# Performance work log

Hardware: AMD Instinct MI355X
Metric: run time of the kernel (lower is better)

The kernel has to match this reference:

```python
import jax, jax.numpy as jnp
import numpy as np

S, G, NMUL, LENF = 730, 4000, 2, 15
NEARZERO = 1e-5

# param bounds (change_param_range: lb + raw*(ub-lb)), raw in [0,1]
HBV_LB = np.array([1., 50., .05, .01, .001, .2, 0., 0., -2.5, .5, 0., 0.], np.float32)
HBV_UB = np.array([6., 1000., .9, .5, .2, 1., 10., 100., 2.5, 10., .1, .2], np.float32)
EXP_LB = np.array([0., 100., 10., 0., 0., -3.], np.float32)
EXP_UB = np.array([.1, 1500., 50., 5., 3., 0.], np.float32)


def _descale(raw, lb, ub):
    # raw: [G, n_par, NMUL]
    return lb[None, :, None] + raw * (ub - lb)[None, :, None]


def _hbv(P, T, PET, ph):
    # ph: [G,12,NMUL]; order: beta fc k0 k1 k2 lp perc uzl tt cfmax cfr cwh
    beta, fc, k0, k1, k2, lp, perc, uzl, tt, cfmax, cfr, cwh = [ph[:, i, :] for i in range(12)]

    def step(carry, inp):
        sp, mw, sm, suz, slz = carry
        p, t, pet = inp
        rain = jnp.where(t >= tt, p, 0.)
        sp = sp + jnp.where(t < tt, p, 0.)
        melt = jnp.minimum(jnp.maximum(cfmax * (t - tt), 0.), sp)
        mw = mw + melt; sp = sp - melt
        refr = jnp.minimum(jnp.maximum(cfr * cfmax * (tt - t), 0.), mw)
        sp = sp + refr; mw = mw - refr
        tosoil = jnp.maximum(mw - cwh * sp, 0.)
        mw = mw - tosoil
        sw = jnp.clip((sm / fc) ** beta, 0., 1.)
        rech = (rain + tosoil) * sw
        sm = sm + rain + tosoil - rech
        excess = jnp.maximum(sm - fc, 0.); sm = sm - excess
        et = jnp.minimum(pet * jnp.clip(sm / (lp * fc), 0., 1.), sm)
        sm = jnp.maximum(sm - et, NEARZERO)
        suz = suz + rech + excess
        pa = jnp.minimum(perc, suz); suz = suz - pa
        q0 = k0 * jnp.maximum(suz - uzl, 0.); suz = suz - q0
        q1 = k1 * suz; suz = suz - q1
        slz = slz + pa
        q2 = k2 * slz; slz = slz - q2
        return (sp, mw, sm, suz, slz), q0 + q1 + q2

    z = jnp.full_like(fc, NEARZERO)
    init = (z, z, 0.5 * fc, z, z)
    _, q = jax.lax.scan(step, init, (P, T, PET))
    return q  # [S,G,NMUL]


def _exphydro(P, T, PET, pe):
    # pe: [G,6,NMUL]; order: f smax qmax df tmax tmin
    f, smax, qmax, df, tmax, tmin = [pe[:, i, :] for i in range(6)]

    def step(carry, inp):
        s0, s1 = carry
        p, t, pet = inp
        ps = jnp.where(t <= tmin, p, 0.)
        pr = p - ps
        melt = jnp.where(t > tmax, jnp.minimum(s0, df * (t - tmax)), 0.)
        s0 = s0 + ps - melt
        s1 = s1 + pr + melt
        qspill = jnp.maximum(s1 - smax, 0.); s1 = s1 - qspill
        et = jnp.minimum(pet * jnp.clip(s1 / smax, 0., 1.), s1); s1 = s1 - et
        qb = jnp.minimum(qmax * jnp.exp(-f * jnp.maximum(smax - s1, 0.)), s1)
        s1 = s1 - qb
        return (s0, s1), qspill + qb

    z = jnp.full_like(smax, NEARZERO)
    init = (z, 0.5 * smax)
    _, q = jax.lax.scan(step, init, (P, T, PET))
    return q  # [S,G,NMUL]


def _uh_gamma(a, b):
    # a,b: [G]; gamma-pdf unit hydrograph, lenF=LENF
    aa = jax.nn.relu(a) + 0.1
    th = jax.nn.relu(b) + 0.5
    t = jnp.arange(LENF, dtype=jnp.float32) + 0.5  # [LENF]
    logw = (-jax.scipy.special.gammaln(aa)[None, :] - aa[None, :] * jnp.log(th)[None, :]
            + (aa - 1.)[None, :] * jnp.log(t)[:, None] - t[:, None] / th[None, :])
    w = jnp.exp(logw)
    return w / w.sum(0, keepdims=True)  # [LENF,G]


def _route(q, w):
    # causal depthwise conv: out[t,g] = sum_k w[k,g] * q[t-k,g]
    qp = jnp.pad(q, ((LENF - 1, 0), (0, 0)))
    out = jnp.zeros_like(q)
    for k in range(LENF):
        out = out + w[k][None, :] * qp[LENF - 1 - k: LENF - 1 - k + q.shape[0]]
    return out


def setup_inputs() -> dict:
    key = jax.random.key(0)
    k1, k2 = jax.random.split(key)
    u = jax.random.uniform(k1, (S, G, 3), dtype=jnp.float32)
    # physical forcing ranges: prcp [0,10] mm/d, tmean [-10,20] C, pet [0,5] mm/d
    x = jnp.stack([u[..., 0] * 10., u[..., 1] * 30. - 10., u[..., 2] * 5.], axis=-1)
    raw_phy_static = jax.random.uniform(k2, (G, 18 * NMUL + 2), dtype=jnp.float32)
    return {"x": x, "raw_phy_static": raw_phy_static}


def reference(x, raw_phy_static):
    # unpack: [G, 18*NMUL] static block + 2 routing params
    static = raw_phy_static[:, :18 * NMUL].reshape(G, 18, NMUL)
    ph = _descale(static[:, :12, :], jnp.asarray(HBV_LB), jnp.asarray(HBV_UB))
    pe = _descale(static[:, 12:, :], jnp.asarray(EXP_LB), jnp.asarray(EXP_UB))
    route = raw_phy_static[:, 18 * NMUL:]
    rout_a = route[:, 0] * 2.9   # bounds [0, 2.9]
    rout_b = route[:, 1] * 6.5   # bounds [0, 6.5]

    P = jnp.broadcast_to(x[:, :, 0, None], (S, G, NMUL))
    T = jnp.broadcast_to(x[:, :, 1, None], (S, G, NMUL))
    PET = jnp.broadcast_to(x[:, :, 2, None], (S, G, NMUL))

    q_hbv = _hbv(P, T, PET, ph)
    q_exp = _exphydro(P, T, PET, pe)
    qsim = 0.5 * (q_hbv.mean(-1) + q_exp.mean(-1))  # blend over models, mean over nmul -> [S,G]

    w = _uh_gamma(rout_a, rout_b)
    return _route(qsim, w)  # [S,G] routed streamflow
```

## Files before the change

### kernel.cpp

```cpp
#include <hip/hip_runtime.h>

#define SS 730
#define GG 4000
#define LENF 15
#define PD 10
#define GPAD 4032
#define TT 10

__global__ __launch_bounds__(64) void hydro_scan(const float* __restrict__ x,
                                                 const float* __restrict__ raw,
                                                 float* __restrict__ qsim) {
    int tid = blockIdx.x * 64 + threadIdx.x;
    int g = tid % GPAD;
    int inst = tid / GPAD;
    if (g >= GG) return;
    int m = inst & 1;
    const float* xg = x + (size_t)g * 3;
    const float* pr = raw + (size_t)g * 38 + m;

    float pb[PD], tb[PD], eb[PD];
#pragma unroll
    for (int j = 0; j < PD; ++j) {
        const float* xn = xg + (size_t)j * (3 * GG);
        pb[j] = xn[0]; tb[j] = xn[1]; eb[j] = xn[2];
    }

    if (inst < 2) {
        float beta  = 1.0f   + pr[0]  * 5.0f;
        float fc    = 50.0f  + pr[2]  * 950.0f;
        float k0    = 0.05f  + pr[4]  * 0.85f;
        float k1    = 0.01f  + pr[6]  * 0.49f;
        float k2    = 0.001f + pr[8]  * 0.199f;
        float lp    = 0.2f   + pr[10] * 0.8f;
        float perc  =          pr[12] * 10.0f;
        float uzl   =          pr[14] * 100.0f;
        float tt    = -2.5f  + pr[16] * 5.0f;
        float cfmax = 0.5f   + pr[18] * 9.5f;
        float cfr   =          pr[20] * 0.1f;
        float cwh   =          pr[22] * 0.2f;
        float invfc   = 1.0f / fc;
        float invlpfc = 1.0f / (lp * fc);
        float cfrcf   = cfr * cfmax;

        float sp = 1e-5f, mw = 1e-5f, sm = 0.5f * fc, suz = 1e-5f, slz = 1e-5f;

        for (int c = 0; c < SS / PD; ++c) {
#pragma unroll
            for (int j = 0; j < PD; ++j) {
                int t = c * PD + j;
                float p = pb[j], tc = tb[j], pet = eb[j];
                {
                    int tn = t + PD; tn = tn < SS ? tn : SS - 1;
                    const float* xn = xg + (size_t)tn * (3 * GG);
                    pb[j] = xn[0]; tb[j] = xn[1]; eb[j] = xn[2];
                }

                float rain = (tc >= tt) ? p : 0.0f;
                float snow = (tc <  tt) ? p : 0.0f;
                sp += snow;
                float melt = fminf(fmaxf(cfmax * (tc - tt), 0.0f), sp);
                mw += melt; sp -= melt;
                float refr = fminf(fmaxf(cfrcf * (tt - tc), 0.0f), mw);
                sp += refr; mw -= refr;
                float tosoil = fmaxf(mw - cwh * sp, 0.0f);
                mw -= tosoil;
                float sw = fminf(exp2f(beta * __log2f(sm * invfc)), 1.0f);
                float rt = rain + tosoil;
                float rech = rt * sw;
                sm += rt - rech;
                float excess = fmaxf(sm - fc, 0.0f);
                sm -= excess;
                float et = fminf(pet * fminf(fmaxf(sm * invlpfc, 0.0f), 1.0f), sm);
                sm = fmaxf(sm - et, 1e-5f);
                suz += rech + excess;
                float pa = fminf(perc, suz);
                suz -= pa;
                float q0 = k0 * fmaxf(suz - uzl, 0.0f);
                suz -= q0;
                float q1 = k1 * suz;
                suz -= q1;
                slz += pa;
                float q2 = k2 * slz;
                slz -= q2;

                atomicAdd(&qsim[t * GG + g], 0.25f * (q0 + q1 + q2));
            }
        }
    } else {
        const float* pe = pr + 24;
        float f    =           pe[0]  * 0.1f;
        float smax = 100.0f  + pe[2]  * 1400.0f;
        float qmax = 10.0f   + pe[4]  * 40.0f;
        float df   =           pe[6]  * 5.0f;
        float tmax =           pe[8]  * 3.0f;
        float tmin = -3.0f   + pe[10] * 3.0f;
        float invsmax = 1.0f / smax;

        float s0 = 1e-5f, s1 = 0.5f * smax;

        for (int c = 0; c < SS / PD; ++c) {
#pragma unroll
            for (int j = 0; j < PD; ++j) {
                int t = c * PD + j;
                float p = pb[j], tc = tb[j], pet = eb[j];
                {
                    int tn = t + PD; tn = tn < SS ? tn : SS - 1;
                    const float* xn = xg + (size_t)tn * (3 * GG);
                    pb[j] = xn[0]; tb[j] = xn[1]; eb[j] = xn[2];
                }

                float ps  = (tc <= tmin) ? p : 0.0f;
                float prr = p - ps;
                float melt = (tc > tmax) ? fminf(s0, df * (tc - tmax)) : 0.0f;
                s0 += ps - melt;
                s1 += prr + melt;
                float qspill = fmaxf(s1 - smax, 0.0f);
                s1 -= qspill;
                float et = fminf(pet * fminf(fmaxf(s1 * invsmax, 0.0f), 1.0f), s1);
                s1 -= et;
                float qb = fminf(qmax * expf(-f * fmaxf(smax - s1, 0.0f)), s1);
                s1 -= qb;

                atomicAdd(&qsim[t * GG + g], 0.25f * (qspill + qb));
            }
        }
    }
}

__global__ __launch_bounds__(256) void hydro_route(const float* __restrict__ qsim,
                                                   const float* __restrict__ raw,
                                                   float* __restrict__ out) {
    int idx = blockIdx.x * 256 + threadIdx.x;
    if (idx >= GG * (SS / TT)) return;
    int g = idx % GG;
    int c = idx / GG;
    int t0 = c * TT;

    float a = raw[(size_t)g * 38 + 36] * 2.9f;
    float b = raw[(size_t)g * 38 + 37] * 6.5f;
    float aa = fmaxf(a, 0.0f) + 0.1f;
    float th = fmaxf(b, 0.0f) + 0.5f;
    float am1 = aa - 1.0f;
    float invth = 1.0f / th;

    const float logt[LENF] = {
        -0.69314718f, 0.40546511f, 0.91629073f, 1.25276297f, 1.50407740f,
         1.70474809f, 1.87180218f, 2.01490302f, 2.14006616f, 2.25129180f,
         2.35137526f, 2.44234704f, 2.52572864f, 2.60268969f, 2.67414865f };

    float w[LENF];
    float s = 0.0f;
#pragma unroll
    for (int k = 0; k < LENF; ++k) {
        float tk = (float)k + 0.5f;
        w[k] = expf(am1 * logt[k] - tk * invth);
        s += w[k];
    }
    float invs = 1.0f / s;

    float v[TT + LENF - 1];
#pragma unroll
    for (int i = 0; i < TT + LENF - 1; ++i) {
        int tp = t0 - (LENF - 1) + i;
        v[i] = (tp >= 0) ? qsim[(size_t)tp * GG + g] : 0.0f;
    }
#pragma unroll
    for (int j = 0; j < TT; ++j) {
        float acc = 0.0f;
#pragma unroll
        for (int k = 0; k < LENF; ++k)
            acc += w[k] * v[j + (LENF - 1) - k];
        out[(size_t)(t0 + j) * GG + g] = acc * invs;
    }
}

extern "C" void kernel_launch(void* const* d_in, const int* in_sizes, int n_in,
                              void* d_out, int out_size, void* d_ws, size_t ws_size,
                              hipStream_t stream) {
    const float* x   = (const float*)d_in[0];
    const float* raw = (const float*)d_in[1];
    float* out  = (float*)d_out;
    float* qsim = (float*)d_ws;

    hipMemsetAsync(qsim, 0, (size_t)SS * GG * sizeof(float), stream);
    hydro_scan<<<(4 * GPAD) / 64, 64, 0, stream>>>(x, raw, qsim);
    hydro_route<<<(GG * (SS / TT) + 255) / 256, 256, 0, stream>>>(qsim, raw, out);
}
```

Baseline: 138.4 us.

## Replace atomic accumulation with per-instance buffers summed in routing kernel

When the workspace is large enough, each of the four model instances writes its runoff to its own buffer with plain stores. The routing kernel then sums the four buffers and applies the 0.25 scale. This removes the memset and the contended float atomics, at the cost of four times the workspace traffic and four loads per routed sample. The scan loop is also restructured with pointer-increment prefetch and a peeled final chunk that drops the clamp.

```diff
diff --git a/kernel.cpp b/kernel.cpp
--- a/kernel.cpp
+++ b/kernel.cpp
@@ -6,7 +6,9 @@
 #define PD 10
 #define GPAD 4032
 #define TT 10
-
+#define QN ((size_t)SS * GG)
+
+template<bool STORE4>
 __global__ __launch_bounds__(64) void hydro_scan(const float* __restrict__ x,
                                                  const float* __restrict__ raw,
                                                  float* __restrict__ qsim) {
@@ -17,6 +19,8 @@
     int m = inst & 1;
     const float* xg = x + (size_t)g * 3;
     const float* pr = raw + (size_t)g * 38 + m;
+
+    float* qp = qsim + (STORE4 ? (size_t)inst * QN : 0) + g;
 
     float pb[PD], tb[PD], eb[PD];
 #pragma unroll
@@ -44,47 +48,54 @@
 
         float sp = 1e-5f, mw = 1e-5f, sm = 0.5f * fc, suz = 1e-5f, slz = 1e-5f;
 
-        for (int c = 0; c < SS / PD; ++c) {
+        auto body = [&](float p, float tc, float pet) -> float {
+            float rain = (tc >= tt) ? p : 0.0f;
+            float snow = (tc <  tt) ? p : 0.0f;
+            sp += snow;
+            float melt = fminf(fmaxf(cfmax * (tc - tt), 0.0f), sp);
+            mw += melt; sp -= melt;
+            float refr = fminf(fmaxf(cfrcf * (tt - tc), 0.0f), mw);
+            sp += refr; mw -= refr;
+            float tosoil = fmaxf(mw - cwh * sp, 0.0f);
+            mw -= tosoil;
+            float sw = fminf(exp2f(beta * __log2f(sm * invfc)), 1.0f);
+            float rt = rain + tosoil;
+            float rech = rt * sw;
+            sm += rt - rech;
+            float excess = fmaxf(sm - fc, 0.0f);
+            sm -= excess;
+            float et = fminf(pet * fminf(fmaxf(sm * invlpfc, 0.0f), 1.0f), sm);
+            sm = fmaxf(sm - et, 1e-5f);
+            suz += rech + excess;
+            float pa = fminf(perc, suz);
+            suz -= pa;
+            float q0 = k0 * fmaxf(suz - uzl, 0.0f);
+            suz -= q0;
+            float q1 = k1 * suz;
+            suz -= q1;
+            slz += pa;
+            float q2 = k2 * slz;
+            slz -= q2;
+            return q0 + q1 + q2;
+        };
+
+        const float* xpre = xg + (size_t)PD * (3 * GG);
+        for (int c = 0; c < SS / PD - 1; ++c) {
 #pragma unroll
             for (int j = 0; j < PD; ++j) {
-                int t = c * PD + j;
                 float p = pb[j], tc = tb[j], pet = eb[j];
-                {
-                    int tn = t + PD; tn = tn < SS ? tn : SS - 1;
-                    const float* xn = xg + (size_t)tn * (3 * GG);
-                    pb[j] = xn[0]; tb[j] = xn[1]; eb[j] = xn[2];
-                }
-
-                float rain = (tc >= tt) ? p : 0.0f;
-                float snow = (tc <  tt) ? p : 0.0f;
-                sp += snow;
-                float melt = fminf(fmaxf(cfmax * (tc - tt), 0.0f), sp);
-                mw += melt; sp -= melt;
-                float refr = fminf(fmaxf(cfrcf * (tt - tc), 0.0f), mw);
-                sp += refr; mw -= refr;
-                float tosoil = fmaxf(mw - cwh * sp, 0.0f);
-                mw -= tosoil;
-                float sw = fminf(exp2f(beta * __log2f(sm * invfc)), 1.0f);
-                float rt = rain + tosoil;
-                float rech = rt * sw;
-                sm += rt - rech;
-                float excess = fmaxf(sm - fc, 0.0f);
-                sm -= excess;
-                float et = fminf(pet * fminf(fmaxf(sm * invlpfc, 0.0f), 1.0f), sm);
-                sm = fmaxf(sm - et, 1e-5f);
-                suz += rech + excess;
-                float pa = fminf(perc, suz);
-                suz -= pa;
-                float q0 = k0 * fmaxf(suz - uzl, 0.0f);
-                suz -= q0;
-                float q1 = k1 * suz;
-                suz -= q1;
-                slz += pa;
-                float q2 = k2 * slz;
-                slz -= q2;
-
-                atomicAdd(&qsim[t * GG + g], 0.25f * (q0 + q1 + q2));
+                pb[j] = xpre[0]; tb[j] = xpre[1]; eb[j] = xpre[2];
+                xpre += 3 * GG;
+                float q = body(p, tc, pet);
+                if (STORE4) *qp = q; else atomicAdd(qp, 0.25f * q);
+                qp += GG;
             }
+        }
+#pragma unroll
+        for (int j = 0; j < PD; ++j) {
+            float q = body(pb[j], tb[j], eb[j]);
+            if (STORE4) *qp = q; else atomicAdd(qp, 0.25f * q);
+            qp += GG;
         }
     } else {
         const float* pe = pr + 24;
@@ -98,35 +109,43 @@
 
         float s0 = 1e-5f, s1 = 0.5f * smax;
 
-        for (int c = 0; c < SS / PD; ++c) {
+        auto body = [&](float p, float tc, float pet) -> float {
+            float ps  = (tc <= tmin) ? p : 0.0f;
+            float prr = p - ps;
+            float melt = (tc > tmax) ? fminf(s0, df * (tc - tmax)) : 0.0f;
+            s0 += ps - melt;
+            s1 += prr + melt;
+            float qspill = fmaxf(s1 - smax, 0.0f);
+            s1 -= qspill;
+            float et = fminf(pet * fminf(fmaxf(s1 * invsmax, 0.0f), 1.0f), s1);
+            s1 -= et;
+            float qb = fminf(qmax * expf(-f * fmaxf(smax - s1, 0.0f)), s1);
+            s1 -= qb;
+            return qspill + qb;
+        };
+
+        const float* xpre = xg + (size_t)PD * (3 * GG);
+        for (int c = 0; c < SS / PD - 1; ++c) {
 #pragma unroll
             for (int j = 0; j < PD; ++j) {
-                int t = c * PD + j;
                 float p = pb[j], tc = tb[j], pet = eb[j];
-                {
-                    int tn = t + PD; tn = tn < SS ? tn : SS - 1;
-                    const float* xn = xg + (size_t)tn * (3 * GG);
-                    pb[j] = xn[0]; tb[j] = xn[1]; eb[j] = xn[2];
-                }
-
-                float ps  = (tc <= tmin) ? p : 0.0f;
-                float prr = p - ps;
-                float melt = (tc > tmax) ? fminf(s0, df * (tc - tmax)) : 0.0f;
-                s0 += ps - melt;
-                s1 += prr + melt;
-                float qspill = fmaxf(s1 - smax, 0.0f);
-                s1 -= qspill;
-                float et = fminf(pet * fminf(fmaxf(s1 * invsmax, 0.0f), 1.0f), s1);
-                s1 -= et;
-                float qb = fminf(qmax * expf(-f * fmaxf(smax - s1, 0.0f)), s1);
-                s1 -= qb;
-
-                atomicAdd(&qsim[t * GG + g], 0.25f * (qspill + qb));
+                pb[j] = xpre[0]; tb[j] = xpre[1]; eb[j] = xpre[2];
+                xpre += 3 * GG;
+                float q = body(p, tc, pet);
+                if (STORE4) *qp = q; else atomicAdd(qp, 0.25f * q);
+                qp += GG;
             }
         }
+#pragma unroll
+        for (int j = 0; j < PD; ++j) {
+            float q = body(pb[j], tb[j], eb[j]);
+            if (STORE4) *qp = q; else atomicAdd(qp, 0.25f * q);
+            qp += GG;
+        }
     }
 }
 
+template<int NB>
 __global__ __launch_bounds__(256) void hydro_route(const float* __restrict__ qsim,
                                                    const float* __restrict__ raw,
                                                    float* __restrict__ out) {
@@ -156,13 +175,19 @@
         w[k] = expf(am1 * logt[k] - tk * invth);
         s += w[k];
     }
-    float invs = 1.0f / s;
+    float scale = (NB == 4 ? 0.25f : 1.0f) / s;
 
     float v[TT + LENF - 1];
 #pragma unroll
     for (int i = 0; i < TT + LENF - 1; ++i) {
         int tp = t0 - (LENF - 1) + i;
-        v[i] = (tp >= 0) ? qsim[(size_t)tp * GG + g] : 0.0f;
+        float sv = 0.0f;
+        if (tp >= 0) {
+            const float* qb = qsim + (size_t)tp * GG + g;
+            sv = qb[0];
+            if (NB == 4) sv += qb[QN] + qb[2 * QN] + qb[3 * QN];
+        }
+        v[i] = sv;
     }
 #pragma unroll
     for (int j = 0; j < TT; ++j) {
@@ -170,7 +195,7 @@
 #pragma unroll
         for (int k = 0; k < LENF; ++k)
             acc += w[k] * v[j + (LENF - 1) - k];
-        out[(size_t)(t0 + j) * GG + g] = acc * invs;
+        out[(size_t)(t0 + j) * GG + g] = acc * scale;
     }
 }
 
@@ -182,7 +207,12 @@
     float* out  = (float*)d_out;
     float* qsim = (float*)d_ws;
 
-    hipMemsetAsync(qsim, 0, (size_t)SS * GG * sizeof(float), stream);
-    hydro_scan<<<(4 * GPAD) / 64, 64, 0, stream>>>(x, raw, qsim);
-    hydro_route<<<(GG * (SS / TT) + 255) / 256, 256, 0, stream>>>(qsim, raw, out);
+    if (ws_size >= 4 * QN * sizeof(float)) {
+        hydro_scan<true><<<(4 * GPAD) / 64, 64, 0, stream>>>(x, raw, qsim);
+        hydro_route<4><<<(GG * (SS / TT) + 255) / 256, 256, 0, stream>>>(qsim, raw, out);
+    } else {
+        hipMemsetAsync(qsim, 0, QN * sizeof(float), stream);
+        hydro_scan<false><<<(4 * GPAD) / 64, 64, 0, stream>>>(x, raw, qsim);
+        hydro_route<1><<<(GG * (SS / TT) + 255) / 256, 256, 0, stream>>>(qsim, raw, out);
+    }
 }
```

Result: faster. 125.9 us (-9.0%).
